# Kernel tuning notes

Hardware: AMD Instinct MI355X
Metric: run time of the kernel (lower is better)

The kernel has to match this reference:

```python
import jax, jax.numpy as jnp
import numpy as np

N, E, C, O, H, W, K = 32, 512, 64, 128, 64, 64, 3


def setup_inputs() -> dict:
    key = jax.random.key(0)
    k1, k2, k3, k4, k5, k6 = jax.random.split(key, 6)
    scale_w = 1.0 / np.sqrt(E)
    return {
        "embedding": jax.random.normal(k1, (N, E), dtype=jnp.float32),
        "images": jax.random.normal(k2, (N, C, H, W), dtype=jnp.float32),
        "w_weight": jax.random.uniform(k3, (O * C * K * K, E), dtype=jnp.float32, minval=-scale_w, maxval=scale_w),
        "w_bias": jax.random.uniform(k4, (O * C * K * K,), dtype=jnp.float32, minval=-scale_w, maxval=scale_w),
        "b_weight": jax.random.uniform(k5, (O, E), dtype=jnp.float32, minval=-scale_w, maxval=scale_w),
        "b_bias": jax.random.uniform(k6, (O,), dtype=jnp.float32, minval=-scale_w, maxval=scale_w),
    }


def reference(embedding, images, w_weight, w_bias, b_weight, b_bias):
    n, c, h, w = images.shape
    o = b_bias.shape[0]
    # per-sample generated filters and biases
    c1_w = embedding @ w_weight.T + w_bias          # [N, O*C*K*K]
    c1_b = embedding @ b_weight.T + b_bias          # [N, O]
    filt = c1_w.reshape(n, o, c, K, K)              # matches torch view(O, C*K*K)
    # im2col equivalent: pad then gather 3x3 shifted views -> [N,C,K,K,H,W]
    xp = jnp.pad(images, ((0, 0), (0, 0), (1, 1), (1, 1)))
    patches = jnp.stack(
        [xp[:, :, i:i + h, j:j + w] for i in range(K) for j in range(K)], axis=2
    ).reshape(n, c, K, K, h, w)
    out = jnp.einsum('nocij,ncijhw->nohw', filt, patches)
    return out + c1_b[:, :, None, None]
```

## Files before the change

kernel.cpp:

```cpp
#include <hip/hip_runtime.h>
#include <hip/hip_bf16.h>

#define N_  32
#define E_  512
#define C_  64
#define O_  128
#define H_  64
#define W_  64
#define CK9 576
#define M_  (O_*CK9)
#define IMGP_ROWB 9216

typedef __bf16 bf16x8 __attribute__((ext_vector_type(8)));
typedef __bf16 bf16x4 __attribute__((ext_vector_type(4)));
typedef float  f32x4  __attribute__((ext_vector_type(4)));

__device__ __forceinline__ void gload_lds16(const void* g, void* l) {
    typedef __attribute__((address_space(1))) const void gvoid;
    typedef __attribute__((address_space(3))) void lvoid;
    __builtin_amdgcn_global_load_lds((gvoid*)g, (lvoid*)l, 16, 0, 0);
}

__global__ __launch_bounds__(256, 3) void producers(
    const float* __restrict__ emb, const float* __restrict__ img,
    const float* __restrict__ w_weight, const float* __restrict__ w_bias,
    const float* __restrict__ b_weight, const float* __restrict__ b_bias,
    __bf16* __restrict__ filt, __bf16* __restrict__ imgp, float* __restrict__ c1b)
{
    __shared__ __align__(16) char smem[51712];
    int bid = blockIdx.x;
    int tid = threadIdx.x;

    if (bid < 576) {
        __bf16* embS = (__bf16*)smem;
        __bf16* wS   = (__bf16*)(smem + 33280);

        int wave = tid >> 6, lane = tid & 63;
        int quad = lane >> 4, l16 = lane & 15;
        int m0 = bid * 128;

        int sub = tid & 15, rbase = tid >> 4;
        const float* wp = w_weight + (size_t)(m0 + rbase) * 512 + sub * 4;
        f32x4 V[8];
#pragma unroll
        for (int q = 0; q < 8; q++)
            V[q] = *reinterpret_cast<const f32x4*>(wp + q * 16 * 512);

#pragma unroll
        for (int i = 0; i < 16; i++) {
            int idx = (i * 256 + tid) * 4;
            int n = idx >> 9, e = idx & 511;
            f32x4 v = *reinterpret_cast<const f32x4*>(emb + n * 512 + e);
            bf16x4 b;
            b[0] = (__bf16)v[0]; b[1] = (__bf16)v[1]; b[2] = (__bf16)v[2]; b[3] = (__bf16)v[3];
            *reinterpret_cast<bf16x4*>(&embS[n * 520 + e]) = b;
        }

        f32x4 acc[2][2];
#pragma unroll
        for (int mi = 0; mi < 2; mi++)
#pragma unroll
            for (int ni = 0; ni < 2; ni++)
                acc[mi][ni] = (f32x4){0.f, 0.f, 0.f, 0.f};

        for (int kk = 0; kk < 8; kk++) {
            int k0 = kk * 64;
            __syncthreads();
#pragma unroll
            for (int q = 0; q < 8; q++) {
                bf16x4 b;
                b[0] = (__bf16)V[q][0]; b[1] = (__bf16)V[q][1];
                b[2] = (__bf16)V[q][2]; b[3] = (__bf16)V[q][3];
                *reinterpret_cast<bf16x4*>(&wS[(rbase + q * 16) * 72 + sub * 4]) = b;
            }
            if (kk < 7) {
#pragma unroll
                for (int q = 0; q < 8; q++)
                    V[q] = *reinterpret_cast<const f32x4*>(wp + q * 16 * 512 + (kk + 1) * 64);
            }
            __syncthreads();

#pragma unroll
            for (int kc = 0; kc < 2; kc++) {
                bf16x8 a0 = *reinterpret_cast<const bf16x8*>(&wS[(wave * 32 + l16) * 72 + kc * 32 + quad * 8]);
                bf16x8 a1 = *reinterpret_cast<const bf16x8*>(&wS[(wave * 32 + 16 + l16) * 72 + kc * 32 + quad * 8]);
                bf16x8 b0 = *reinterpret_cast<const bf16x8*>(&embS[l16 * 520 + k0 + kc * 32 + quad * 8]);
                bf16x8 b1 = *reinterpret_cast<const bf16x8*>(&embS[(16 + l16) * 520 + k0 + kc * 32 + quad * 8]);
                acc[0][0] = __builtin_amdgcn_mfma_f32_16x16x32_bf16(a0, b0, acc[0][0], 0, 0, 0);
                acc[0][1] = __builtin_amdgcn_mfma_f32_16x16x32_bf16(a0, b1, acc[0][1], 0, 0, 0);
                acc[1][0] = __builtin_amdgcn_mfma_f32_16x16x32_bf16(a1, b0, acc[1][0], 0, 0, 0);
                acc[1][1] = __builtin_amdgcn_mfma_f32_16x16x32_bf16(a1, b1, acc[1][1], 0, 0, 0);
            }
        }

#pragma unroll
        for (int mi = 0; mi < 2; mi++) {
#pragma unroll
            for (int r = 0; r < 4; r++) {
                int m = m0 + wave * 32 + mi * 16 + quad * 4 + r;
                int o = m / 576;
                int rem = m - o * 576;
                int c = rem / 9;
                int t = rem - c * 9;
                int kp = t * 64 + c;
                size_t base = ((size_t)(kp >> 3) << 10) + ((size_t)o << 3) + (kp & 7);
                float bias = w_bias[m];
#pragma unroll
                for (int ni = 0; ni < 2; ni++) {
                    int n = ni * 16 + l16;
                    filt[(size_t)n * M_ + base] = (__bf16)(acc[mi][ni][r] + bias);
                }
            }
        }
    } else if (bid < 2688) {
        __bf16* ldsT = (__bf16*)smem;
        int blk = bid - 576;
        int n = blk / 66, hh = blk - n * 66;
        char* dst = (char*)imgp + ((size_t)n * 66 + hh) * IMGP_ROWB;

        bf16x8 zero = {(__bf16)0.f, (__bf16)0.f, (__bf16)0.f, (__bf16)0.f,
                       (__bf16)0.f, (__bf16)0.f, (__bf16)0.f, (__bf16)0.f};

        if (hh == 0 || hh == 65) {
#pragma unroll
            for (int j = 0; j < 3; j++) {
                int u = j * 256 + tid;
                if (u < 576) *reinterpret_cast<bf16x8*>(dst + u * 16) = zero;
            }
            return;
        }

        int h = hh - 1;
        const float* srcn = img + (size_t)n * (C_ * H_ * W_) + h * 64;
#pragma unroll
        for (int i = 0; i < 4; i++) {
            int idx = i * 256 + tid;
            int c = idx >> 4, wq = (idx & 15) * 4;
            f32x4 v = *reinterpret_cast<const f32x4*>(srcn + (size_t)c * 4096 + wq);
#pragma unroll
            for (int j = 0; j < 4; j++)
                ldsT[(wq + j) * 72 + c] = (__bf16)v[j];
        }
        __syncthreads();

#pragma unroll
        for (int j = 0; j < 3; j++) {
            int u = j * 256 + tid;
            if (u < 576) {
                int col = u >> 3, s = u & 7;
                bf16x8 val = zero;
                if (col >= 1 && col <= 64) {
                    int b = s ^ (col & 7);
                    val = *reinterpret_cast<const bf16x8*>(&ldsT[(col - 1) * 72 + b * 8]);
                }
                *reinterpret_cast<bf16x8*>(dst + u * 16) = val;
            }
        }
    } else {
        int wave = tid >> 6, lane = tid & 63;
        int wid = ((bid - 2688) << 2) + wave;
        int n = wid >> 7, o = wid & 127;
        const float* e = emb + (size_t)n * E_ + lane * 8;
        const float* b = b_weight + (size_t)o * E_ + lane * 8;
        f32x4 e0 = *reinterpret_cast<const f32x4*>(e);
        f32x4 e1 = *reinterpret_cast<const f32x4*>(e + 4);
        f32x4 w0 = *reinterpret_cast<const f32x4*>(b);
        f32x4 w1 = *reinterpret_cast<const f32x4*>(b + 4);
        float s = e0[0]*w0[0] + e0[1]*w0[1] + e0[2]*w0[2] + e0[3]*w0[3]
                + e1[0]*w1[0] + e1[1]*w1[1] + e1[2]*w1[2] + e1[3]*w1[3];
#pragma unroll
        for (int off = 32; off; off >>= 1) s += __shfl_xor(s, off, 64);
        if (lane == 0) c1b[wid] = s + b_bias[o];
    }
}

__global__ __launch_bounds__(256, 2) void conv_gemm(
    const __bf16* __restrict__ imgp, const __bf16* __restrict__ filt,
    const float* __restrict__ c1b, float* __restrict__ out)
{
    __shared__ __align__(16) char smemc[36864];
    __bf16* slab  = (__bf16*)smemc;
    float*  ep    = (float*)smemc;
    char*   slabB = smemc;
    (void)slab;

    int tid  = threadIdx.x;
    int wave = tid >> 6, lane = tid & 63;
    int quad = lane >> 4, l16 = lane & 15;

    int blk = blockIdx.x;
    int n     = ((blk & 7) << 2) + ((blk >> 3) & 3);
    int strip = blk >> 5;

    const __bf16* fN   = filt + (size_t)n * M_;
    const char*   srcN = (const char*)imgp + (size_t)n * 66 * IMGP_ROWB;
    int oB = wave * 32 + l16;

    float biasv[2][4];
#pragma unroll
    for (int mi = 0; mi < 2; mi++)
#pragma unroll
        for (int r = 0; r < 4; r++)
            biasv[mi][r] = c1b[(n << 7) + wave * 32 + mi * 16 + quad * 4 + r];

    int colA[4][3][2];
#pragma unroll
    for (int cb = 0; cb < 4; cb++)
#pragma unroll
        for (int tj = 0; tj < 3; tj++) {
            int col = cb * 16 + l16 + tj;
#pragma unroll
            for (int ck = 0; ck < 2; ck++)
                colA[cb][tj][ck] = col * 128 + (((quad + ck * 4) ^ (col & 7)) << 4);
        }

    for (int pt2 = 0; pt2 < 2; pt2++) {
        int pt = strip * 2 + pt2;
        int h0 = pt * 2;

        __syncthreads();

        const char* src = srcN + (size_t)h0 * IMGP_ROWB;
#pragma unroll
        for (int j = 0; j < 9; j++)
            gload_lds16(src + (j * 256 + tid) * 16,
                        slabB + (j * 256 + wave * 64) * 16);
        __syncthreads();

        f32x4 acc[2][8];
#pragma unroll
        for (int mi = 0; mi < 2; mi++)
#pragma unroll
            for (int ni = 0; ni < 8; ni++)
                acc[mi][ni] = (f32x4){0.f, 0.f, 0.f, 0.f};

#pragma unroll
        for (int tj = 0; tj < 3; tj++) {
#pragma unroll
            for (int ck = 0; ck < 2; ck++) {
                bf16x8 aR2[2][3];
#pragma unroll
                for (int mi = 0; mi < 2; mi++)
#pragma unroll
                    for (int di = 0; di < 3; di++) {
                        int kk = 2 * (di * 3 + tj) + ck;
                        aR2[mi][di] = *reinterpret_cast<const bf16x8*>(
                            fN + (((kk * 4 + quad) << 10) + ((oB + mi * 16) << 3)));
                    }
                bf16x8 b2[4][4];
#pragma unroll
                for (int row = 0; row < 4; row++)
#pragma unroll
                    for (int cb = 0; cb < 4; cb++)
                        b2[row][cb] = *reinterpret_cast<const bf16x8*>(
                            slabB + row * IMGP_ROWB + colA[cb][tj][ck]);
#pragma unroll
                for (int di = 0; di < 3; di++)
#pragma unroll
                    for (int mi = 0; mi < 2; mi++)
#pragma unroll
                        for (int lh = 0; lh < 2; lh++)
#pragma unroll
                            for (int cb = 0; cb < 4; cb++)
                                acc[mi][(lh << 2) | cb] = __builtin_amdgcn_mfma_f32_16x16x32_bf16(
                                    aR2[mi][di], b2[lh + di][cb], acc[mi][(lh << 2) | cb], 0, 0, 0);
            }
        }

#pragma unroll
        for (int mi = 0; mi < 2; mi++) {
            __syncthreads();
#pragma unroll
            for (int ni = 0; ni < 8; ni++) {
                int lh = ni >> 2, cb = ni & 3;
#pragma unroll
                for (int r = 0; r < 4; r++)
                    ep[wave * 2112 + (quad * 4 + r) * 132 + lh * 64 + cb * 16 + l16] =
                        acc[mi][ni][r] + biasv[mi][r];
            }
            __syncthreads();
#pragma unroll
            for (int u = 0; u < 8; u++) {
                int idx = u * 256 + tid;
                int row = idx >> 5, s16 = idx & 31;
                int w2 = row >> 4, ol = row & 15;
                f32x4 v = *reinterpret_cast<const f32x4*>(&ep[w2 * 2112 + ol * 132 + s16 * 4]);
                int o = w2 * 32 + mi * 16 + ol;
                *reinterpret_cast<f32x4*>(
                    out + (((size_t)(n << 7) + o) << 12) + (pt << 7) + s16 * 4) = v;
            }
        }
    }
}

extern "C" void kernel_launch(void* const* d_in, const int* in_sizes, int n_in,
                              void* d_out, int out_size, void* d_ws, size_t ws_size,
                              hipStream_t stream)
{
    (void)in_sizes; (void)n_in; (void)out_size; (void)ws_size;
    const float* emb      = (const float*)d_in[0];
    const float* images   = (const float*)d_in[1];
    const float* w_weight = (const float*)d_in[2];
    const float* w_bias   = (const float*)d_in[3];
    const float* b_weight = (const float*)d_in[4];
    const float* b_bias   = (const float*)d_in[5];
    float* out = (float*)d_out;

    __bf16* filt = (__bf16*)d_ws;
    float*  c1b  = (float*)((char*)d_ws + (size_t)N_ * M_ * 2);
    __bf16* imgp = (__bf16*)((char*)d_ws + (size_t)N_ * M_ * 2 + 16384);

    producers<<<dim3(3712), dim3(256), 0, stream>>>(
        emb, images, w_weight, w_bias, b_weight, b_bias, filt, imgp, c1b);
    conv_gemm<<<dim3(512), dim3(256), 0, stream>>>(imgp, filt, c1b, out);
}
```

Before: 306.0 us.

## Stream weights directly into MFMA fragments and split conv strips across more blocks

The filter-generating GEMM now loads the fp32 weight rows straight from global memory into registers and converts them to bf16 MFMA A-fragments. This drops the LDS staging buffer and its per-iteration barriers, which shrinks LDS use and raises the occupancy target. The conv GEMM no longer loops over two row-pairs per block: grid size doubles to 1024 blocks with one tile each and launch bounds rise to 4 waves per SIMD. The image transpose load indexing is also reshuffled. The direct weight loads are less coalesced than the staged path, and the conv kernel now has to fit in a tighter register budget.

After: 317.3 us. 3.7% more time.

```diff
diff --git a/kernel.cpp b/kernel.cpp
--- a/kernel.cpp
+++ b/kernel.cpp
@@ -21,30 +21,21 @@
     __builtin_amdgcn_global_load_lds((gvoid*)g, (lvoid*)l, 16, 0, 0);
 }
 
-__global__ __launch_bounds__(256, 3) void producers(
+__global__ __launch_bounds__(256, 4) void producers(
     const float* __restrict__ emb, const float* __restrict__ img,
     const float* __restrict__ w_weight, const float* __restrict__ w_bias,
     const float* __restrict__ b_weight, const float* __restrict__ b_bias,
     __bf16* __restrict__ filt, __bf16* __restrict__ imgp, float* __restrict__ c1b)
 {
-    __shared__ __align__(16) char smem[51712];
+    __shared__ __align__(16) char smem[33280];
     int bid = blockIdx.x;
     int tid = threadIdx.x;
 
     if (bid < 576) {
         __bf16* embS = (__bf16*)smem;
-        __bf16* wS   = (__bf16*)(smem + 33280);
-
         int wave = tid >> 6, lane = tid & 63;
         int quad = lane >> 4, l16 = lane & 15;
         int m0 = bid * 128;
-
-        int sub = tid & 15, rbase = tid >> 4;
-        const float* wp = w_weight + (size_t)(m0 + rbase) * 512 + sub * 4;
-        f32x4 V[8];
-#pragma unroll
-        for (int q = 0; q < 8; q++)
-            V[q] = *reinterpret_cast<const f32x4*>(wp + q * 16 * 512);
 
 #pragma unroll
         for (int i = 0; i < 16; i++) {
@@ -55,6 +46,10 @@
             b[0] = (__bf16)v[0]; b[1] = (__bf16)v[1]; b[2] = (__bf16)v[2]; b[3] = (__bf16)v[3];
             *reinterpret_cast<bf16x4*>(&embS[n * 520 + e]) = b;
         }
+        __syncthreads();
+
+        const float* a0p = w_weight + (size_t)(m0 + wave * 32 + l16) * 512 + quad * 8;
+        const float* a1p = a0p + 16 * 512;
 
         f32x4 acc[2][2];
 #pragma unroll
@@ -63,34 +58,28 @@
             for (int ni = 0; ni < 2; ni++)
                 acc[mi][ni] = (f32x4){0.f, 0.f, 0.f, 0.f};
 
-        for (int kk = 0; kk < 8; kk++) {
-            int k0 = kk * 64;
-            __syncthreads();
-#pragma unroll
-            for (int q = 0; q < 8; q++) {
-                bf16x4 b;
-                b[0] = (__bf16)V[q][0]; b[1] = (__bf16)V[q][1];
-                b[2] = (__bf16)V[q][2]; b[3] = (__bf16)V[q][3];
-                *reinterpret_cast<bf16x4*>(&wS[(rbase + q * 16) * 72 + sub * 4]) = b;
-            }
-            if (kk < 7) {
-#pragma unroll
-                for (int q = 0; q < 8; q++)
-                    V[q] = *reinterpret_cast<const f32x4*>(wp + q * 16 * 512 + (kk + 1) * 64);
-            }
-            __syncthreads();
-
-#pragma unroll
-            for (int kc = 0; kc < 2; kc++) {
-                bf16x8 a0 = *reinterpret_cast<const bf16x8*>(&wS[(wave * 32 + l16) * 72 + kc * 32 + quad * 8]);
-                bf16x8 a1 = *reinterpret_cast<const bf16x8*>(&wS[(wave * 32 + 16 + l16) * 72 + kc * 32 + quad * 8]);
-                bf16x8 b0 = *reinterpret_cast<const bf16x8*>(&embS[l16 * 520 + k0 + kc * 32 + quad * 8]);
-                bf16x8 b1 = *reinterpret_cast<const bf16x8*>(&embS[(16 + l16) * 520 + k0 + kc * 32 + quad * 8]);
-                acc[0][0] = __builtin_amdgcn_mfma_f32_16x16x32_bf16(a0, b0, acc[0][0], 0, 0, 0);
-                acc[0][1] = __builtin_amdgcn_mfma_f32_16x16x32_bf16(a0, b1, acc[0][1], 0, 0, 0);
-                acc[1][0] = __builtin_amdgcn_mfma_f32_16x16x32_bf16(a1, b0, acc[1][0], 0, 0, 0);
-                acc[1][1] = __builtin_amdgcn_mfma_f32_16x16x32_bf16(a1, b1, acc[1][1], 0, 0, 0);
-            }
+#pragma unroll
+        for (int kk = 0; kk < 16; kk++) {
+            int k0 = kk * 32;
+            f32x4 v00 = *reinterpret_cast<const f32x4*>(a0p + k0);
+            f32x4 v01 = *reinterpret_cast<const f32x4*>(a0p + k0 + 4);
+            f32x4 v10 = *reinterpret_cast<const f32x4*>(a1p + k0);
+            f32x4 v11 = *reinterpret_cast<const f32x4*>(a1p + k0 + 4);
+            bf16x8 a0, a1;
+            a0[0] = (__bf16)v00[0]; a0[1] = (__bf16)v00[1];
+            a0[2] = (__bf16)v00[2]; a0[3] = (__bf16)v00[3];
+            a0[4] = (__bf16)v01[0]; a0[5] = (__bf16)v01[1];
+            a0[6] = (__bf16)v01[2]; a0[7] = (__bf16)v01[3];
+            a1[0] = (__bf16)v10[0]; a1[1] = (__bf16)v10[1];
+            a1[2] = (__bf16)v10[2]; a1[3] = (__bf16)v10[3];
+            a1[4] = (__bf16)v11[0]; a1[5] = (__bf16)v11[1];
+            a1[6] = (__bf16)v11[2]; a1[7] = (__bf16)v11[3];
+            bf16x8 b0 = *reinterpret_cast<const bf16x8*>(&embS[l16 * 520 + k0 + quad * 8]);
+            bf16x8 b1 = *reinterpret_cast<const bf16x8*>(&embS[(16 + l16) * 520 + k0 + quad * 8]);
+            acc[0][0] = __builtin_amdgcn_mfma_f32_16x16x32_bf16(a0, b0, acc[0][0], 0, 0, 0);
+            acc[0][1] = __builtin_amdgcn_mfma_f32_16x16x32_bf16(a0, b1, acc[0][1], 0, 0, 0);
+            acc[1][0] = __builtin_amdgcn_mfma_f32_16x16x32_bf16(a1, b0, acc[1][0], 0, 0, 0);
+            acc[1][1] = __builtin_amdgcn_mfma_f32_16x16x32_bf16(a1, b1, acc[1][1], 0, 0, 0);
         }
 
 #pragma unroll
@@ -132,14 +121,13 @@
 
         int h = hh - 1;
         const float* srcn = img + (size_t)n * (C_ * H_ * W_) + h * 64;
+        int c0 = (tid & 15) * 4, w0 = (tid >> 4) * 4;
 #pragma unroll
         for (int i = 0; i < 4; i++) {
-            int idx = i * 256 + tid;
-            int c = idx >> 4, wq = (idx & 15) * 4;
-            f32x4 v = *reinterpret_cast<const f32x4*>(srcn + (size_t)c * 4096 + wq);
+            f32x4 v = *reinterpret_cast<const f32x4*>(srcn + (size_t)(c0 + i) * 4096 + w0);
 #pragma unroll
             for (int j = 0; j < 4; j++)
-                ldsT[(wq + j) * 72 + c] = (__bf16)v[j];
+                ldsT[(w0 + j) * 72 + c0 + i] = (__bf16)v[j];
         }
         __syncthreads();
 
@@ -174,23 +162,22 @@
     }
 }
 
-__global__ __launch_bounds__(256, 2) void conv_gemm(
+__global__ __launch_bounds__(256, 4) void conv_gemm(
     const __bf16* __restrict__ imgp, const __bf16* __restrict__ filt,
     const float* __restrict__ c1b, float* __restrict__ out)
 {
     __shared__ __align__(16) char smemc[36864];
-    __bf16* slab  = (__bf16*)smemc;
-    float*  ep    = (float*)smemc;
-    char*   slabB = smemc;
-    (void)slab;
+    float* ep    = (float*)smemc;
+    char*  slabB = smemc;
 
     int tid  = threadIdx.x;
     int wave = tid >> 6, lane = tid & 63;
     int quad = lane >> 4, l16 = lane & 15;
 
     int blk = blockIdx.x;
-    int n     = ((blk & 7) << 2) + ((blk >> 3) & 3);
-    int strip = blk >> 5;
+    int n  = ((blk & 7) << 2) + ((blk >> 3) & 3);
+    int pt = blk >> 5;
+    int h0 = pt * 2;
 
     const __bf16* fN   = filt + (size_t)n * M_;
     const char*   srcN = (const char*)imgp + (size_t)n * 66 * IMGP_ROWB;
@@ -203,6 +190,12 @@
         for (int r = 0; r < 4; r++)
             biasv[mi][r] = c1b[(n << 7) + wave * 32 + mi * 16 + quad * 4 + r];
 
+    const char* src = srcN + (size_t)h0 * IMGP_ROWB;
+#pragma unroll
+    for (int j = 0; j < 9; j++)
+        gload_lds16(src + (j * 256 + tid) * 16,
+                    slabB + (j * 256 + wave * 64) * 16);
+
     int colA[4][3][2];
 #pragma unroll
     for (int cb = 0; cb < 4; cb++)
@@ -214,81 +207,69 @@
                 colA[cb][tj][ck] = col * 128 + (((quad + ck * 4) ^ (col & 7)) << 4);
         }
 
-    for (int pt2 = 0; pt2 < 2; pt2++) {
-        int pt = strip * 2 + pt2;
-        int h0 = pt * 2;
-
-        __syncthreads();
-
-        const char* src = srcN + (size_t)h0 * IMGP_ROWB;
-#pragma unroll
-        for (int j = 0; j < 9; j++)
-            gload_lds16(src + (j * 256 + tid) * 16,
-                        slabB + (j * 256 + wave * 64) * 16);
-        __syncthreads();
-
-        f32x4 acc[2][8];
-#pragma unroll
-        for (int mi = 0; mi < 2; mi++)
-#pragma unroll
-            for (int ni = 0; ni < 8; ni++)
-                acc[mi][ni] = (f32x4){0.f, 0.f, 0.f, 0.f};
-
-#pragma unroll
-        for (int tj = 0; tj < 3; tj++) {
-#pragma unroll
-            for (int ck = 0; ck < 2; ck++) {
-                bf16x8 aR2[2][3];
+    f32x4 acc[2][8];
+#pragma unroll
+    for (int mi = 0; mi < 2; mi++)
+#pragma unroll
+        for (int ni = 0; ni < 8; ni++)
+            acc[mi][ni] = (f32x4){0.f, 0.f, 0.f, 0.f};
+
+    __syncthreads();
+
+#pragma unroll
+    for (int tj = 0; tj < 3; tj++) {
+#pragma unroll
+        for (int ck = 0; ck < 2; ck++) {
+            bf16x8 aR2[2][3];
+#pragma unroll
+            for (int mi = 0; mi < 2; mi++)
+#pragma unroll
+                for (int di = 0; di < 3; di++) {
+                    int kk = 2 * (di * 3 + tj) + ck;
+                    aR2[mi][di] = *reinterpret_cast<const bf16x8*>(
+                        fN + (((kk * 4 + quad) << 10) + ((oB + mi * 16) << 3)));
+                }
+            bf16x8 b2[4][4];
+#pragma unroll
+            for (int row = 0; row < 4; row++)
+#pragma unroll
+                for (int cb = 0; cb < 4; cb++)
+                    b2[row][cb] = *reinterpret_cast<const bf16x8*>(
+                        slabB + row * IMGP_ROWB + colA[cb][tj][ck]);
+#pragma unroll
+            for (int di = 0; di < 3; di++)
 #pragma unroll
                 for (int mi = 0; mi < 2; mi++)
 #pragma unroll
-                    for (int di = 0; di < 3; di++) {
-                        int kk = 2 * (di * 3 + tj) + ck;
-                        aR2[mi][di] = *reinterpret_cast<const bf16x8*>(
-                            fN + (((kk * 4 + quad) << 10) + ((oB + mi * 16) << 3)));
-                    }
-                bf16x8 b2[4][4];
-#pragma unroll
-                for (int row = 0; row < 4; row++)
-#pragma unroll
-                    for (int cb = 0; cb < 4; cb++)
-                        b2[row][cb] = *reinterpret_cast<const bf16x8*>(
-                            slabB + row * IMGP_ROWB + colA[cb][tj][ck]);
-#pragma unroll
-                for (int di = 0; di < 3; di++)
-#pragma unroll
-                    for (int mi = 0; mi < 2; mi++)
-#pragma unroll
-                        for (int lh = 0; lh < 2; lh++)
-#pragma unroll
-                            for (int cb = 0; cb < 4; cb++)
-                                acc[mi][(lh << 2) | cb] = __builtin_amdgcn_mfma_f32_16x16x32_bf16(
-                                    aR2[mi][di], b2[lh + di][cb], acc[mi][(lh << 2) | cb], 0, 0, 0);
-            }
-        }
-
-#pragma unroll
-        for (int mi = 0; mi < 2; mi++) {
-            __syncthreads();
-#pragma unroll
-            for (int ni = 0; ni < 8; ni++) {
-                int lh = ni >> 2, cb = ni & 3;
-#pragma unroll
-                for (int r = 0; r < 4; r++)
-                    ep[wave * 2112 + (quad * 4 + r) * 132 + lh * 64 + cb * 16 + l16] =
-                        acc[mi][ni][r] + biasv[mi][r];
-            }
-            __syncthreads();
-#pragma unroll
-            for (int u = 0; u < 8; u++) {
-                int idx = u * 256 + tid;
-                int row = idx >> 5, s16 = idx & 31;
-                int w2 = row >> 4, ol = row & 15;
-                f32x4 v = *reinterpret_cast<const f32x4*>(&ep[w2 * 2112 + ol * 132 + s16 * 4]);
-                int o = w2 * 32 + mi * 16 + ol;
-                *reinterpret_cast<f32x4*>(
-                    out + (((size_t)(n << 7) + o) << 12) + (pt << 7) + s16 * 4) = v;
-            }
+                    for (int lh = 0; lh < 2; lh++)
+#pragma unroll
+                        for (int cb = 0; cb < 4; cb++)
+                            acc[mi][(lh << 2) | cb] = __builtin_amdgcn_mfma_f32_16x16x32_bf16(
+                                aR2[mi][di], b2[lh + di][cb], acc[mi][(lh << 2) | cb], 0, 0, 0);
+        }
+    }
+
+#pragma unroll
+    for (int mi = 0; mi < 2; mi++) {
+        __syncthreads();
+#pragma unroll
+        for (int ni = 0; ni < 8; ni++) {
+            int lh = ni >> 2, cb = ni & 3;
+#pragma unroll
+            for (int r = 0; r < 4; r++)
+                ep[wave * 2112 + (quad * 4 + r) * 132 + lh * 64 + cb * 16 + l16] =
+                    acc[mi][ni][r] + biasv[mi][r];
+        }
+        __syncthreads();
+#pragma unroll
+        for (int u = 0; u < 8; u++) {
+            int idx = u * 256 + tid;
+            int row = idx >> 5, s16 = idx & 31;
+            int w2 = row >> 4, ol = row & 15;
+            f32x4 v = *reinterpret_cast<const f32x4*>(&ep[w2 * 2112 + ol * 132 + s16 * 4]);
+            int o = w2 * 32 + mi * 16 + ol;
+            *reinterpret_cast<f32x4*>(
+                out + (((size_t)(n << 7) + o) << 12) + (pt << 7) + s16 * 4) = v;
         }
     }
 }
@@ -312,5 +293,5 @@
 
     producers<<<dim3(3712), dim3(256), 0, stream>>>(
         emb, images, w_weight, w_bias, b_weight, b_bias, filt, imgp, c1b);
-    conv_gemm<<<dim3(512), dim3(256), 0, stream>>>(imgp, filt, c1b, out);
-}
+    conv_gemm<<<dim3(1024), dim3(256), 0, stream>>>(imgp, filt, c1b, out);
+}
```
